# Kernel tuning notes

Measured on AMD Instinct MI355X. Metric: run time of the kernel, lower is better.

The kernel has to match this reference:

```python
import jax, jax.numpy as jnp
import numpy as np
from math import sqrt

NUM_CLASSES = 21
TOP_K = 200
CONF_THRESH = 0.01
NMS_THRESH = 0.45
VAR0, VAR1 = 0.1, 0.2
FMAPS = [19, 10, 5, 3, 2, 1]
INPUT_SIZE = 300
STEPS = [16, 32, 64, 100, 150, 300]
MIN_SIZES = [60, 105, 150, 195, 240, 285]
MAX_SIZES = [105, 150, 195, 240, 285, 330]
ASPECT_RATIOS = [[2, 3]] * 6


def _create_priorbox():
    # Faithful numpy port of create_priorbox (runs once at setup).
    mean = []
    for k, f in enumerate(FMAPS):
        f_k = INPUT_SIZE / STEPS[k]
        s_k = MIN_SIZES[k] / INPUT_SIZE
        s_kp = sqrt(s_k * (MAX_SIZES[k] / INPUT_SIZE))
        for i in range(f):
            for j in range(f):
                cx = (j + 0.5) / f_k
                cy = (i + 0.5) / f_k
                mean.append([cx, cy, s_k, s_k])
                mean.append([cx, cy, s_kp, s_kp])
                for ar in ASPECT_RATIOS[k]:
                    r = sqrt(ar)
                    mean.append([cx, cy, s_k * r, s_k / r])
                    mean.append([cx, cy, s_k / r, s_k * r])
    return np.clip(np.asarray(mean, dtype=np.float32), 0.0, 1.0)  # [3000, 4]


def setup_inputs() -> dict:
    key = jax.random.key(0)
    k1, k2 = jax.random.split(key)
    B, P, C = 8, 3000, NUM_CLASSES
    loc_data = jax.random.normal(k1, (B, P, 4), jnp.float32)
    conf_data = jax.random.uniform(k2, (B, P, C), jnp.float32)  # post-softmax-like probs
    priors = jnp.asarray(_create_priorbox())
    return {"loc_data": loc_data, "conf_data": conf_data, "priors": priors}


def _decode(loc, priors):
    # SSD box decode: center-offset form -> corner form. loc, priors: [P, 4]
    cxcy = priors[:, :2] + loc[:, :2] * VAR0 * priors[:, 2:]
    wh = priors[:, 2:] * jnp.exp(loc[:, 2:] * VAR1)
    xy1 = cxcy - 0.5 * wh
    return jnp.concatenate([xy1, xy1 + wh], axis=-1)  # [P, 4] (x1, y1, x2, y2)


def _iou_matrix(b):
    # b: [P, 4] corner-form boxes -> [P, P] pairwise IoU
    area = (b[:, 2] - b[:, 0]) * (b[:, 3] - b[:, 1])
    lt = jnp.maximum(b[:, None, :2], b[None, :, :2])
    rb = jnp.minimum(b[:, None, 2:], b[None, :, 2:])
    wh = jnp.clip(rb - lt, 0.0)
    inter = wh[..., 0] * wh[..., 1]
    union = area[:, None] + area[None, :] - inter
    return inter / jnp.maximum(union, 1e-12)


def _nms_one_class(scores, boxes):
    # scores: [P], boxes: [P, 4]. Greedy hard NMS over threshold-passing boxes,
    # kept detections (in score order) padded to TOP_K rows of [score, x1, y1, x2, y2].
    P = scores.shape[0]
    valid = scores > CONF_THRESH
    s = jnp.where(valid, scores, -jnp.inf)
    order = jnp.argsort(-s)  # descending by score; invalid sorted last
    ss = s[order]
    sb = boxes[order]
    sv = valid[order]
    iou = _iou_matrix(sb)  # [P, P]
    idx = jnp.arange(P)

    def body(i, keep):
        sup = keep[i] & (iou[i] > NMS_THRESH) & (idx > i)
        return keep & ~sup

    keep = jax.lax.stop_gradient(jax.lax.fori_loop(0, P, body, sv))
    # first TOP_K kept candidates, preserving score order
    sel = jnp.argsort(jnp.where(keep, idx, idx + P))[:TOP_K]
    ok = keep[sel]
    out_s = jnp.where(ok, ss[sel], 0.0)
    out_b = jnp.where(ok[:, None], sb[sel], 0.0)
    return jnp.concatenate([out_s[:, None], out_b], axis=-1)  # [TOP_K, 5]


def _per_image(loc, conf, priors):
    boxes = _decode(loc, priors)  # [P, 4]
    cls_scores = conf.T[1:]  # skip background class 0 -> [C-1, P]
    dets = jax.vmap(lambda s: _nms_one_class(s, boxes))(cls_scores)  # [C-1, TOP_K, 5]
    bg = jnp.zeros((1, TOP_K, 5), dets.dtype)
    return jnp.concatenate([bg, dets], axis=0)  # [C, TOP_K, 5]


def reference(loc_data, conf_data, priors):
    # lax.map over batch keeps peak memory to one image's IoU matrices.
    # NOTE: the original's final flt[(rank < top_k)].fill_(0) is a no-op in
    # PyTorch (advanced indexing returns a copy), so output is returned as-is.
    out = jax.lax.map(lambda lc: _per_image(lc[0], lc[1], priors), (loc_data, conf_data))
    return out  # [B, NUM_CLASSES, TOP_K, 5]
```

## Files before the change

### kernel.cpp

```cpp
#include <hip/hip_runtime.h>
#include <math.h>

#pragma clang fp contract(off)

#define PNUM    3000
#define NCLS    21
#define TOPK    200
#define BLOCK   1024
#define CHUNK   1024
#define NMS_T   0.45f
#define LO_BITS 0x3C23D70Bu
#define HI_BITS 0x3F800001u
#define MAXKEEP (TOPK + 64)

__device__ __constant__ unsigned LADDER[15] = {
    0x3F333333u, 0x3F266666u, 0x3F19999Au, 0x3F0CCCCDu, 0x3F000000u,
    0x3EE66666u, 0x3ECCCCCDu, 0x3EB33333u, 0x3E99999Au, 0x3E800000u,
    0x3E4CCCCDu, 0x3E19999Au, 0x3DCCCCCDu, 0x3D4CCCCDu, LO_BITS };

__device__ __forceinline__ float iou_f(float4 a, float aa, float4 b, float ab) {
    float ltx = fmaxf(a.x, b.x);
    float lty = fmaxf(a.y, b.y);
    float rbx = fminf(a.z, b.z);
    float rby = fminf(a.w, b.w);
    float iw  = fmaxf(rbx - ltx, 0.0f);
    float ih  = fmaxf(rby - lty, 0.0f);
    float inter = iw * ih;
    float uni   = aa + ab - inter;
    return inter / fmaxf(uni, 1e-12f);
}

__global__ __launch_bounds__(BLOCK) void ssd_nms_kernel(
    const float* __restrict__ loc,
    const float* __restrict__ conf,
    const float* __restrict__ priors,
    float* __restrict__ out)
{
    const int c   = blockIdx.x;
    const int b   = blockIdx.y;
    const int tid = threadIdx.x;

    float* outbase = out + ((size_t)(b * NCLS + c)) * (TOPK * 5);

    if (c == 0) {
        for (int i = tid; i < TOPK * 5; i += BLOCK) outbase[i] = 0.0f;
        return;
    }

    __shared__ unsigned long long s_bufA[CHUNK];
    __shared__ unsigned long long s_bufB[CHUNK];
    __shared__ float4             s_box[CHUNK];
    __shared__ float              s_area[CHUNK];
    __shared__ float              s_score[CHUNK];
    __shared__ float4             s_kb[MAXKEEP];
    __shared__ float              s_ka[MAXKEEP];
    __shared__ unsigned long long s_supp[64];
    __shared__ int                s_supc[64];
    __shared__ int                s_wcnt[16];
    __shared__ int s_m, s_cnt, s_done;

    const int lane = tid & 63;
    const int wav  = tid >> 6;

    unsigned hb[4];
    const float* confb = conf + ((size_t)b * PNUM) * NCLS + c;
    #pragma unroll
    for (int q = 0; q < 4; ++q) {
        int i = tid + (q << 10);
        unsigned h = 0u;
        if (i < PNUM) {
            float s = confb[(size_t)i * NCLS];
            if (s > 0.01f) h = __float_as_uint(s);
        }
        hb[q] = h;
    }
    if (tid < 64) { s_supp[lane] = 0ull; s_supc[lane] = 0; }
    if (tid == 0) { s_cnt = 0; s_done = 0; }

    unsigned Thi = HI_BITS;
    int rung = 0;
    bool done = false;

    for (;;) {
        unsigned T = LADDER[rung];

        __syncthreads();
        if (tid == 0) s_m = 0;
        s_bufA[tid] = 0ull;
        __syncthreads();
        #pragma unroll
        for (int q = 0; q < 4; ++q) {
            unsigned sb = hb[q];
            bool p = (sb >= T && sb < Thi);
            unsigned long long bal = __ballot(p);
            int wb = 0;
            if (lane == 0 && bal) wb = atomicAdd(&s_m, (int)__popcll(bal));
            wb = __shfl(wb, 0);
            if (p) {
                int dst = wb + (int)__popcll(bal & ((1ull << lane) - 1ull));
                if (dst < CHUNK) {
                    int i = tid + (q << 10);
                    s_bufA[dst] = ((unsigned long long)sb << 32) | (unsigned)(~i);
                }
            }
        }
        __syncthreads();
        int M = s_m;

        if (M > CHUNK) {
            unsigned lo = T + 1, hi = Thi;
            while (lo < hi) {
                unsigned mid = lo + ((hi - lo) >> 1);
                __syncthreads();
                int c2 = 0;
                #pragma unroll
                for (int q = 0; q < 4; ++q)
                    c2 += (int)__popcll(__ballot(hb[q] >= mid && hb[q] < Thi));
                if (lane == 0) s_wcnt[wav] = c2;
                __syncthreads();
                int n = 0;
                #pragma unroll
                for (int w = 0; w < 16; ++w) n += s_wcnt[w];
                if (n <= CHUNK) hi = mid; else lo = mid + 1;
            }
            T = hi;
            __syncthreads();
            int wc = 0;
            #pragma unroll
            for (int q = 0; q < 4; ++q)
                wc += (int)__popcll(__ballot(hb[q] >= T && hb[q] < Thi));
            if (lane == 0) s_wcnt[wav] = wc;
            s_bufA[tid] = 0ull;
            __syncthreads();
            int wbase = 0; M = 0;
            #pragma unroll
            for (int w = 0; w < 16; ++w) {
                int v = s_wcnt[w];
                M += v;
                if (w < wav) wbase += v;
            }
            int base = wbase;
            #pragma unroll
            for (int q = 0; q < 4; ++q) {
                unsigned sb = hb[q];
                bool p = (sb >= T && sb < Thi);
                unsigned long long bal = __ballot(p);
                if (p) {
                    int dst = base + (int)__popcll(bal & ((1ull << lane) - 1ull));
                    int i = tid + (q << 10);
                    s_bufA[dst] = ((unsigned long long)sb << 32) | (unsigned)(~i);
                }
                base += (int)__popcll(bal);
            }
            __syncthreads();
        }

        if (M == 0) {
            if (T <= LO_BITS) break;
            Thi = T; if (T > LADDER[rung]) {} else rung++;
            continue;
        }

        unsigned N = 64;
        while (N < (unsigned)M) N <<= 1;
        unsigned long long key = s_bufA[tid];
        int parity = 0;
        for (unsigned k = 2; k <= N; k <<= 1) {
            for (unsigned j = k >> 1; j > 0; j >>= 1) {
                unsigned long long pk;
                if (j >= 64) {
                    unsigned long long* buf = parity ? s_bufB : s_bufA;
                    buf[tid] = key;
                    __syncthreads();
                    pk = buf[tid ^ j];
                    parity ^= 1;
                } else {
                    pk = __shfl_xor(key, (int)j, 64);
                }
                bool takeMax  = (((tid & j) == 0) == ((tid & k) == 0));
                bool pGreater = pk > key;
                if (takeMax == pGreater) key = pk;
            }
        }

        if (key != 0ull) {
            unsigned idx = ~(unsigned)key;
            float4 l  = ((const float4*)loc)[(size_t)b * PNUM + idx];
            float4 pr = ((const float4*)priors)[idx];
            float cx = pr.x + l.x * 0.1f * pr.z;
            float cy = pr.y + l.y * 0.1f * pr.w;
            float w  = pr.z * expf(l.z * 0.2f);
            float h  = pr.w * expf(l.w * 0.2f);
            float x1 = cx - 0.5f * w;
            float y1 = cy - 0.5f * h;
            float x2 = x1 + w;
            float y2 = y1 + h;
            s_box[tid]   = make_float4(x1, y1, x2, y2);
            s_area[tid]  = (x2 - x1) * (y2 - y1);
            s_score[tid] = __uint_as_float((unsigned)(key >> 32));
        }
        __syncthreads();

        int pos = 0;
        while (pos < M) {
            int bn  = M - pos; if (bn > 64) bn = 64;
            int cnt = s_cnt;

            if (lane < bn) {
                float4 bL = s_box[pos + lane];
                float  aL = s_area[pos + lane];
                bool bad = false;
                #pragma unroll 2
                for (int K = wav; K < cnt; K += 16)
                    bad |= (iou_f(s_kb[K], s_ka[K], bL, aL) > NMS_T);
                if (bad) s_supc[lane] = 1;
                unsigned long long bits = 0ull;
                int M0 = wav << 2;
                #pragma unroll
                for (int q2 = 0; q2 < 4; ++q2) {
                    int Mi = M0 + q2;
                    if (Mi < lane) {
                        if (iou_f(s_box[pos + Mi], s_area[pos + Mi], bL, aL) > NMS_T)
                            bits |= (1ull << Mi);
                    }
                }
                if (bits) atomicOr(&s_supp[lane], bits);
            }
            __syncthreads();

            if (tid < 64) {
                unsigned long long own      = s_supp[lane];
                unsigned long long deadmask = __ballot(s_supc[lane] != 0);
                bool alive = (lane < bn) && !((deadmask >> lane) & 1ull);
                unsigned long long kept = __ballot(alive && own == 0ull);
                unsigned long long todo = __ballot(alive && own != 0ull);
                while (todo) {
                    int L = __ffsll(todo) - 1;
                    unsigned long long ownL = __shfl(own, L, 64);
                    if (!(ownL & kept)) kept |= 1ull << L;
                    todo &= todo - 1;
                }
                int keptN = (int)__popcll(kept);
                bool me   = (kept >> lane) & 1ull;
                int krank = (int)__popcll(kept & ((1ull << lane) - 1ull));
                if (me) {
                    int kid = cnt + krank;
                    float4 bx = s_box[pos + lane];
                    s_kb[kid] = bx;
                    s_ka[kid] = s_area[pos + lane];
                    if (kid < TOPK) {
                        float* o = outbase + (size_t)kid * 5;
                        o[0] = s_score[pos + lane];
                        o[1] = bx.x; o[2] = bx.y; o[3] = bx.z; o[4] = bx.w;
                    }
                }
                s_supp[lane] = 0ull;
                s_supc[lane] = 0;
                if (lane == 0) {
                    s_cnt  = cnt + keptN;
                    s_done = (cnt + keptN >= TOPK) ? 1 : 0;
                }
            }
            __syncthreads();
            if (s_done) { done = true; break; }
            pos += bn;
        }

        if (done) break;
        if (T <= LO_BITS) break;
        Thi = T;
        while (rung < 14 && LADDER[rung] >= T) rung++;
    }

    const int cf = s_cnt < TOPK ? s_cnt : TOPK;
    for (int r = cf + tid; r < TOPK; r += BLOCK) {
        float* o = outbase + (size_t)r * 5;
        o[0] = 0.f; o[1] = 0.f; o[2] = 0.f; o[3] = 0.f; o[4] = 0.f;
    }
}

extern "C" void kernel_launch(void* const* d_in, const int* in_sizes, int n_in,
                              void* d_out, int out_size, void* d_ws, size_t ws_size,
                              hipStream_t stream) {
    const float* loc    = (const float*)d_in[0];
    const float* conf   = (const float*)d_in[1];
    const float* priors = (const float*)d_in[2];
    float* out          = (float*)d_out;
    const int B = in_sizes[0] / (PNUM * 4);
    dim3 grid(NCLS, B);
    ssd_nms_kernel<<<grid, BLOCK, 0, stream>>>(loc, conf, priors, out);
}
```

Measured before the change: 91.70 us.

## Resolve NMS chunk redundantly in every wave to drop a barrier per chunk

Each wave now writes its per-lane suppression bits and a ballot of dead lanes into double-buffered shared arrays instead of using shared atomics. Every wave then reduces these and resolves the 64-candidate chunk itself, so the keep count stays in registers and the second __syncthreads per chunk is removed. The serial per-lane resolve loop is replaced by a parallel ballot fixpoint iteration. The cost is redundant resolve work in all 16 waves and extra shared-memory reads for the 16-way reduction.

```diff
diff --git a/kernel.cpp b/kernel.cpp
--- a/kernel.cpp
+++ b/kernel.cpp
@@ -54,10 +54,10 @@
     __shared__ float              s_score[CHUNK];
     __shared__ float4             s_kb[MAXKEEP];
     __shared__ float              s_ka[MAXKEEP];
-    __shared__ unsigned long long s_supp[64];
-    __shared__ int                s_supc[64];
+    __shared__ unsigned long long s_supT[2][16][64];
+    __shared__ unsigned long long s_deadT[2][16];
     __shared__ int                s_wcnt[16];
-    __shared__ int s_m, s_cnt, s_done;
+    __shared__ int s_m;
 
     const int lane = tid & 63;
     const int wav  = tid >> 6;
@@ -74,11 +74,10 @@
         }
         hb[q] = h;
     }
-    if (tid < 64) { s_supp[lane] = 0ull; s_supc[lane] = 0; }
-    if (tid == 0) { s_cnt = 0; s_done = 0; }
 
     unsigned Thi = HI_BITS;
     int rung = 0;
+    int cnt = 0;
     bool done = false;
 
     for (;;) {
@@ -157,7 +156,8 @@
 
         if (M == 0) {
             if (T <= LO_BITS) break;
-            Thi = T; if (T > LADDER[rung]) {} else rung++;
+            Thi = T;
+            while (rung < 14 && LADDER[rung] >= T) rung++;
             continue;
         }
 
@@ -202,68 +202,74 @@
         __syncthreads();
 
         int pos = 0;
+        int parityR = 0;
         while (pos < M) {
-            int bn  = M - pos; if (bn > 64) bn = 64;
-            int cnt = s_cnt;
-
-            if (lane < bn) {
-                float4 bL = s_box[pos + lane];
-                float  aL = s_area[pos + lane];
+            int bn = M - pos; if (bn > 64) bn = 64;
+
+            {
+                unsigned long long bits = 0ull;
                 bool bad = false;
-                #pragma unroll 2
-                for (int K = wav; K < cnt; K += 16)
-                    bad |= (iou_f(s_kb[K], s_ka[K], bL, aL) > NMS_T);
-                if (bad) s_supc[lane] = 1;
-                unsigned long long bits = 0ull;
-                int M0 = wav << 2;
-                #pragma unroll
-                for (int q2 = 0; q2 < 4; ++q2) {
-                    int Mi = M0 + q2;
-                    if (Mi < lane) {
-                        if (iou_f(s_box[pos + Mi], s_area[pos + Mi], bL, aL) > NMS_T)
-                            bits |= (1ull << Mi);
+                if (lane < bn) {
+                    float4 bL = s_box[pos + lane];
+                    float  aL = s_area[pos + lane];
+                    #pragma unroll 2
+                    for (int K = wav; K < cnt; K += 16)
+                        bad |= (iou_f(s_kb[K], s_ka[K], bL, aL) > NMS_T);
+                    int M0 = wav << 2;
+                    #pragma unroll
+                    for (int q2 = 0; q2 < 4; ++q2) {
+                        int Mi = M0 + q2;
+                        if (Mi < lane) {
+                            if (iou_f(s_box[pos + Mi], s_area[pos + Mi], bL, aL) > NMS_T)
+                                bits |= (1ull << Mi);
+                        }
                     }
                 }
-                if (bits) atomicOr(&s_supp[lane], bits);
-            }
-            __syncthreads();
-
-            if (tid < 64) {
-                unsigned long long own      = s_supp[lane];
-                unsigned long long deadmask = __ballot(s_supc[lane] != 0);
-                bool alive = (lane < bn) && !((deadmask >> lane) & 1ull);
-                unsigned long long kept = __ballot(alive && own == 0ull);
-                unsigned long long todo = __ballot(alive && own != 0ull);
-                while (todo) {
-                    int L = __ffsll(todo) - 1;
-                    unsigned long long ownL = __shfl(own, L, 64);
-                    if (!(ownL & kept)) kept |= 1ull << L;
-                    todo &= todo - 1;
-                }
-                int keptN = (int)__popcll(kept);
-                bool me   = (kept >> lane) & 1ull;
+                s_supT[parityR][wav][lane] = bits;
+                unsigned long long db = __ballot(bad);
+                if (lane == 0) s_deadT[parityR][wav] = db;
+            }
+            __syncthreads();
+
+            unsigned long long own = 0ull, dead = 0ull;
+            #pragma unroll
+            for (int w = 0; w < 16; ++w) {
+                own  |= s_supT[parityR][w][lane];
+                dead |= s_deadT[parityR][w];
+            }
+            unsigned long long aliveM =
+                ((bn == 64) ? ~0ull : ((1ull << bn) - 1ull)) & ~dead;
+            bool alive = (aliveM >> lane) & 1ull;
+            unsigned long long kept  = __ballot(alive && own == 0ull);
+            unsigned long long undec = aliveM & ~kept;
+            while (undec) {
+                bool inU = (undec >> lane) & 1ull;
+                bool dd  = inU && (own & kept) != 0ull;
+                bool kk  = inU && (own & kept) == 0ull && (own & undec) == 0ull;
+                unsigned long long nd = __ballot(dd);
+                unsigned long long nk = __ballot(kk);
+                kept  |= nk;
+                undec &= ~(nd | nk);
+            }
+
+            int keptN = (int)__popcll(kept);
+            if ((kept >> lane) & 1ull) {
                 int krank = (int)__popcll(kept & ((1ull << lane) - 1ull));
-                if (me) {
-                    int kid = cnt + krank;
-                    float4 bx = s_box[pos + lane];
-                    s_kb[kid] = bx;
-                    s_ka[kid] = s_area[pos + lane];
-                    if (kid < TOPK) {
-                        float* o = outbase + (size_t)kid * 5;
-                        o[0] = s_score[pos + lane];
-                        o[1] = bx.x; o[2] = bx.y; o[3] = bx.z; o[4] = bx.w;
-                    }
-                }
-                s_supp[lane] = 0ull;
-                s_supc[lane] = 0;
-                if (lane == 0) {
-                    s_cnt  = cnt + keptN;
-                    s_done = (cnt + keptN >= TOPK) ? 1 : 0;
-                }
-            }
-            __syncthreads();
-            if (s_done) { done = true; break; }
+                int kid = cnt + krank;
+                int sl  = pos + lane;
+                float4 bx = s_box[sl];
+                s_kb[kid] = bx;
+                s_ka[kid] = s_area[sl];
+                if (wav == 0 && kid < TOPK) {
+                    float* o = outbase + (size_t)kid * 5;
+                    o[0] = s_score[sl];
+                    o[1] = bx.x; o[2] = bx.y; o[3] = bx.z; o[4] = bx.w;
+                }
+            }
+            cnt += keptN;
+            if (cnt >= TOPK) { done = true; break; }
             pos += bn;
+            parityR ^= 1;
         }
 
         if (done) break;
@@ -272,7 +278,8 @@
         while (rung < 14 && LADDER[rung] >= T) rung++;
     }
 
-    const int cf = s_cnt < TOPK ? s_cnt : TOPK;
+    __syncthreads();
+    const int cf = cnt < TOPK ? cnt : TOPK;
     for (int r = cf + tid; r < TOPK; r += BLOCK) {
         float* o = outbase + (size_t)r * 5;
         o[0] = 0.f; o[1] = 0.f; o[2] = 0.f; o[3] = 0.f; o[4] = 0.f;
```

New measurement: 93.13 us. No clear change (+1.6%).
